# Performance work log

Hardware: AMD Instinct MI355X
Metric: run time of the kernel (lower is better)

## Reference

```python
import jax, jax.numpy as jnp
import numpy as np

C = 256

def conv1x1(x, w, b):
    # pointwise Conv3d(kernel=1): out-channel d from in-channel c
    return jnp.einsum('blhwc,dc->blhwd', x, w) + b

def setup_inputs() -> dict:
    key = jax.random.key(0)
    ks = jax.random.split(key, 20)
    inp = {
        'x': jax.random.normal(ks[0], (2, 8, 64, 64, C + 3), jnp.float32),
        'mask': jnp.ones((2, 8, 64, 64), dtype=bool),
        'spatial_correction_matrix': jax.random.normal(ks[1], (2, 8, 4, 4), jnp.float32),
    }
    scale = 1.0 / np.sqrt(C)
    names = ['sq', 'sk', 'sv', 'tq', 'tk', 'tv']
    for i, n in enumerate(names):
        inp[n + '_w'] = jax.random.normal(ks[2 + 2 * i], (C, C), jnp.float32) * scale
        inp[n + '_b'] = jax.random.normal(ks[3 + 2 * i], (C,), jnp.float32) * 0.01
    inp['s_gamma'] = jax.random.normal(ks[14], (1,), jnp.float32) * 0.1
    inp['t_gamma'] = jax.random.normal(ks[15], (1,), jnp.float32) * 0.1
    return inp

def reference(x, mask, spatial_correction_matrix,
              sq_w, sq_b, sk_w, sk_b, sv_w, sv_b, s_gamma,
              tq_w, tq_b, tk_w, tk_b, tv_w, tv_b, t_gamma):
    x_s = x[..., :-3]                      # (B,L,H,W,C)
    B, L, H, W, Ch = x_s.shape
    prev = x_s                             # last_time == None -> last_time = x.detach()
    HW = H * W

    # ---- SpatialAttention: channel-attention (CxC) per (B,L) slice ----
    q = jnp.transpose(conv1x1(x_s, sq_w, sq_b), (0, 1, 4, 2, 3)).reshape(B * L, Ch, HW)
    k = jnp.transpose(conv1x1(x_s, sk_w, sk_b), (0, 1, 4, 2, 3)).reshape(B * L, Ch, HW)
    attn = jax.nn.softmax(jnp.einsum('bcs,bds->bcd', q, k), axis=-1)   # (BL,C,C)
    v = jnp.transpose(conv1x1(x_s, sv_w, sv_b), (0, 1, 4, 2, 3)).reshape(B * L, Ch, HW)
    out = jnp.einsum('bds,bcd->bsc', v, attn).reshape(B, L, H, W, Ch)
    x1 = s_gamma * out + x_s

    # ---- TemporalAttention: query from x1, key/value from prev ----
    q2 = jnp.transpose(conv1x1(x1, tq_w, tq_b), (0, 1, 4, 2, 3)).reshape(B * L, Ch, HW)
    # key: permute(0,2,1,4,3) swaps H/W before flatten (faithful to source)
    k2 = jnp.transpose(conv1x1(prev, tk_w, tk_b), (0, 1, 4, 3, 2)).reshape(B * L, Ch, HW)
    attn2 = jax.nn.softmax(jnp.einsum('bcs,bds->bcd', q2, k2), axis=-1)
    # value: reshape of (B,C,L,H,W)-contiguous tensor into (B*L,C,HW) scrambles C/L (faithful)
    v2 = jnp.transpose(conv1x1(prev, tv_w, tv_b), (0, 4, 1, 2, 3)).reshape(B * L, Ch, HW)
    out2 = jnp.einsum('bds,bcd->bsc', v2, attn2).reshape(B, L, H, W, Ch)
    x2 = t_gamma * out2 + x1
    return x2
```

## Files before the change

### kernel.cpp

```cpp
#include <hip/hip_runtime.h>
#include <stdint.h>


#define S4 4096
#define CH 256

typedef __attribute__((ext_vector_type(8))) short bf16x8;
typedef __attribute__((ext_vector_type(4))) float f32x4;

static __device__ __forceinline__ float bf2f(unsigned short u){
  union { unsigned int i; float f; } v; v.i = ((unsigned int)u) << 16; return v.f;
}
static __device__ __forceinline__ unsigned short f2bf(float f){
  union { float f; unsigned int i; } v; v.f = f;
  unsigned int x = v.i;
  x += 0x7fffu + ((x >> 16) & 1u);
  return (unsigned short)(x >> 16);
}
static __device__ __forceinline__ void gload16(const void* g, void* l){
  __builtin_amdgcn_global_load_lds((const __attribute__((address_space(1))) void*)g,
                                   (__attribute__((address_space(3))) void*)l, 16, 0, 0);
}


__global__ void k_xprep(const float* __restrict__ x,
                        unsigned short* __restrict__ xhi,
                        unsigned short* __restrict__ xlo){
  int row = blockIdx.x;
  int c   = threadIdx.x;
  float v = x[(size_t)row*259 + c];
  unsigned short h = f2bf(v);
  xhi[(size_t)row*256 + c] = h;
  xlo[(size_t)row*256 + c] = f2bf(v - bf2f(h));
}

__global__ void k_wprep(const float* __restrict__ w0, const float* __restrict__ w1,
                        const float* __restrict__ w2, const float* __restrict__ w3,
                        const float* __restrict__ w4, const float* __restrict__ w5,
                        unsigned short* __restrict__ whi, unsigned short* __restrict__ wlo,
                        unsigned short* __restrict__ wvthi, unsigned short* __restrict__ wvtlo){
  int i = blockIdx.x*256 + threadIdx.x;
  int mat = i >> 16; int off = i & 65535;
  if (mat < 6){
    const float* src = mat==0?w0:mat==1?w1:mat==2?w2:mat==3?w3:mat==4?w4:w5;
    float v = src[off];
    unsigned short h = f2bf(v);
    whi[i] = h;
    wlo[i] = f2bf(v - bf2f(h));
  } else {
    int e = off >> 8, d = off & 255;
    float v = w2[d*256 + e];
    unsigned short h = f2bf(v);
    wvthi[off] = h;
    wvtlo[off] = f2bf(v - bf2f(h));
  }
}


__global__ void k_colsum(const float* __restrict__ x, float* __restrict__ ups){
  int bl = blockIdx.x, ch = blockIdx.y, e = threadIdx.x;
  float s = 0.f;
  for (int i=0;i<128;++i){
    int row = bl*4096 + ch*128 + i;
    s += x[(size_t)row*259 + e];
  }
  ups[(bl*32 + ch)*256 + e] = s;
}

__global__ void k_vecfin(const float* __restrict__ ups, float* __restrict__ u){
  int bl = blockIdx.x, e = threadIdx.x;
  float s = 0.f;
  for (int ch=0;ch<32;++ch) s += ups[(bl*32+ch)*256 + e];
  u[bl*256 + e] = s;
}

__global__ void k_vecs1(const float* __restrict__ sq_w, const float* __restrict__ sq_b,
                        const float* __restrict__ sk_w, const float* __restrict__ tk_w,
                        const float* __restrict__ u,
                        float* __restrict__ wqu, float* __restrict__ wku, float* __restrict__ wtku){
  int bl = blockIdx.x, mat = blockIdx.y;
  const float* W = mat==0? sq_w : mat==1? sk_w : tk_w;
  int l = threadIdx.x & 63, w = threadIdx.x >> 6;
  const float* ub = u + bl*256;
  for (int i=0;i<64;++i){
    int c = w*64 + i;
    float s = 0.f;
    #pragma unroll
    for (int j=0;j<4;++j) s += W[c*256 + l + 64*j] * ub[l + 64*j];
    #pragma unroll
    for (int off=32; off; off>>=1) s += __shfl_xor(s, off, 64);
    if (l==0){
      if (mat==0) wqu [bl*256+c] = s + 4096.f*sq_b[c];
      else if (mat==1) wku [bl*256+c] = s;
      else wtku[bl*256+c] = s;
    }
  }
}

__global__ void k_vecs2a(const unsigned short* __restrict__ a1hi, const unsigned short* __restrict__ a1lo,
                         const float* __restrict__ bv, const float* __restrict__ M1,
                         const float* __restrict__ u,
                         float* __restrict__ c1, float* __restrict__ m1u){
  int bl = blockIdx.x, mat = blockIdx.y;
  int l = threadIdx.x & 63, w = threadIdx.x >> 6;
  for (int i=0;i<64;++i){
    int c = w*64 + i;
    float s = 0.f;
    if (mat==0){
      #pragma unroll
      for (int j=0;j<4;++j){
        long o = (long)bl*65536 + c*256 + l + 64*j;
        s += (bf2f(a1hi[o]) + bf2f(a1lo[o])) * bv[l + 64*j];
      }
    } else {
      #pragma unroll
      for (int j=0;j<4;++j)
        s += M1[(long)bl*65536 + c*256 + l + 64*j] * u[bl*256 + l + 64*j];
    }
    #pragma unroll
    for (int off=32; off; off>>=1) s += __shfl_xor(s, off, 64);
    if (l==0){
      if (mat==0) c1 [bl*256+c] = s;
      else        m1u[bl*256+c] = s;
    }
  }
}

__global__ void k_vecs2b(const float* __restrict__ u, const float* __restrict__ m1u,
                         const float* __restrict__ c1, const float* __restrict__ s_g,
                         const float* __restrict__ tq_w, const float* __restrict__ tq_b,
                         float* __restrict__ b1eff, float* __restrict__ wtqh){
  __shared__ float h1[256];
  int bl = blockIdx.x, tid = threadIdx.x;
  float g = s_g[0];
  float b1 = g * c1[bl*256 + tid];
  b1eff[bl*256 + tid] = b1;
  h1[tid] = u[bl*256+tid] + g*m1u[bl*256+tid] + 4096.f*b1;
  __syncthreads();
  int l = tid & 63, w = tid >> 6;
  for (int i=0;i<64;++i){
    int c = w*64 + i;
    float s = 0.f;
    #pragma unroll
    for (int j=0;j<4;++j) s += tq_w[c*256 + l + 64*j] * h1[l + 64*j];
    #pragma unroll
    for (int off=32; off; off>>=1) s += __shfl_xor(s, off, 64);
    if (l==0) wtqh[bl*256+c] = s + 4096.f*tq_b[c];
  }
}

__global__ void k_w1eff(const float* __restrict__ M1, const float* __restrict__ s_g,
                        unsigned short* __restrict__ w1hi, unsigned short* __restrict__ w1lo){
  int bl = blockIdx.y;
  int idx = blockIdx.x*256 + threadIdx.x;
  int c = idx >> 8, e = idx & 255;
  float v = ((c==e)?1.f:0.f) + s_g[0]*M1[(long)bl*65536 + idx];
  unsigned short h = f2bf(v);
  w1hi[(long)bl*65536 + idx] = h;
  w1lo[(long)bl*65536 + idx] = f2bf(v - bf2f(h));
}

__global__ void k_gcomb(const float* __restrict__ Gp,
                        unsigned short* __restrict__ ghi, unsigned short* __restrict__ glo){
  int bl = blockIdx.y;
  int idx = blockIdx.x*256 + threadIdx.x;
  float s = 0.f;
  #pragma unroll
  for (int p=0;p<4;++p) s += Gp[(long)(bl*4+p)*65536 + idx];
  unsigned short h = f2bf(s);
  ghi[(long)bl*65536 + idx] = h;
  glo[(long)bl*65536 + idx] = f2bf(s - bf2f(h));
}

template<int MODE>
__global__ void k_softmax(const float* __restrict__ lp, const float* __restrict__ gp,
                          unsigned short* __restrict__ ahi, unsigned short* __restrict__ alo){
  int tid = threadIdx.x;
  int l = tid & 63, w = tid >> 6;
  int row = blockIdx.x*4 + w;
  int bl = row >> 8, c = row & 255;
  const float* b0 = lp + (long)bl*65536 + c*256 + l*4;
  float4 v = *(const float4*)b0;
  float m = fmaxf(fmaxf(v.x,v.y), fmaxf(v.z,v.w));
  #pragma unroll
  for (int off=32; off; off>>=1) m = fmaxf(m, __shfl_xor(m, off, 64));
  float e0=__expf(v.x-m), e1=__expf(v.y-m), e2=__expf(v.z-m), e3=__expf(v.w-m);
  float s = e0+e1+e2+e3;
  #pragma unroll
  for (int off=32; off; off>>=1) s += __shfl_xor(s, off, 64);
  float inv = 1.f/s;
  if (MODE==1) inv *= gp[0];
  float p[4] = {e0*inv, e1*inv, e2*inv, e3*inv};
  long o = (long)bl*65536 + c*256 + l*4;
  ushort4 hh;
  hh.x=f2bf(p[0]); hh.y=f2bf(p[1]); hh.z=f2bf(p[2]); hh.w=f2bf(p[3]);
  *(ushort4*)(ahi + o) = hh;
  if (MODE==0){
    ushort4 ll;
    ll.x=f2bf(p[0]-bf2f(hh.x)); ll.y=f2bf(p[1]-bf2f(hh.y));
    ll.z=f2bf(p[2]-bf2f(hh.z)); ll.w=f2bf(p[3]-bf2f(hh.w));
    *(ushort4*)(alo + o) = ll;
  }
}


template<bool SPLIT,int OUT_MODE>
__global__ __launch_bounds__(256) void k_gemm(
  const unsigned short* __restrict__ Ahi, const unsigned short* __restrict__ Alo,
  long Abl, int Ars,
  const unsigned short* __restrict__ Bhi, const unsigned short* __restrict__ Blo,
  long Bbl, int Brs,
  const float* __restrict__ bias,
  const float* __restrict__ r1a, int r1as, const float* __restrict__ r1b, int r1bs,
  const float* __restrict__ r2a, int r2as, const float* __restrict__ r2b, int r2bs,
  unsigned short* __restrict__ O16a, unsigned short* __restrict__ O16b,
  float* __restrict__ O32, long Obl, int Ors)
{
  constexpr int LDSZ = SPLIT ? 65536 : 32768;
  __shared__ char lds[LDSZ];
  char* ldsAh = lds;
  char* ldsAl = lds + 16384;
  char* ldsBh = lds + (SPLIT ? 32768 : 16384);
  char* ldsBl = lds + 49152;

  const int tid = threadIdx.x;
  const int l   = tid & 63;
  const int wid = tid >> 6;
  const int wm  = wid >> 1, wn = wid & 1;
  const int lm  = l & 15, lk = l >> 4;
  const int fm  = wm*64, fn = wn*64;
  const int bl  = blockIdx.z;
  const int m0  = blockIdx.x * 128;
  const int n0  = blockIdx.y * 128;

  f32x4 acc[4][4];
  #pragma unroll
  for (int i=0;i<4;++i)
    #pragma unroll
    for (int j=0;j<4;++j) acc[i][j] = (f32x4){0.f,0.f,0.f,0.f};

  for (int kt = 0; kt < 4; ++kt) {
    const int kq = kt << 6;
    #pragma unroll
    for (int it=0; it<4; ++it) {
      int idx = it*256 + tid;
      int r = idx >> 3;
      int kb = ((idx & 7) << 4) ^ ((r & 7) << 4);
      long ga = (long)bl*Abl + (long)(m0 + r)*Ars + kq + (kb >> 1);
      gload16(Ahi + ga, ldsAh + idx*16);
      if (SPLIT) gload16(Alo + ga, ldsAl + idx*16);
      long gb = (long)bl*Bbl + (long)(n0 + r)*Brs + kq + (kb >> 1);
      gload16(Bhi + gb, ldsBh + idx*16);
      if (SPLIT) gload16(Blo + gb, ldsBl + idx*16);
    }
    __syncthreads();
    #pragma unroll
    for (int kk=0; kk<2; ++kk) {
      bf16x8 ah[4], al_[4];
      #pragma unroll
      for (int i=0;i<4;++i) {
        int r = fm + i*16 + lm;
        int kb = ((kk<<6) + (lk<<4)) ^ ((r & 7) << 4);
        ah[i] = *(const bf16x8*)(ldsAh + r*128 + kb);
        if (SPLIT) al_[i] = *(const bf16x8*)(ldsAl + r*128 + kb);
      }
      #pragma unroll
      for (int j=0;j<4;++j) {
        int r = fn + j*16 + lm;
        int kb = ((kk<<6) + (lk<<4)) ^ ((r & 7) << 4);
        bf16x8 bh = *(const bf16x8*)(ldsBh + r*128 + kb);
        bf16x8 bl8;
        if (SPLIT) bl8 = *(const bf16x8*)(ldsBl + r*128 + kb);
        #pragma unroll
        for (int i=0;i<4;++i) {
          acc[i][j] = __builtin_amdgcn_mfma_f32_16x16x32_bf16(ah[i], bh, acc[i][j], 0, 0, 0);
          if (SPLIT) {
            acc[i][j] = __builtin_amdgcn_mfma_f32_16x16x32_bf16(ah[i], bl8, acc[i][j], 0, 0, 0);
            acc[i][j] = __builtin_amdgcn_mfma_f32_16x16x32_bf16(al_[i], bh, acc[i][j], 0, 0, 0);
          }
        }
      }
    }
    __syncthreads();
  }

  float* ldsF = (float*)lds;
  #pragma unroll
  for (int chv=0; chv<4; ++chv) {
    __syncthreads();
    if (wm == (chv >> 1)) {
      #pragma unroll
      for (int i2=0;i2<2;++i2) {
        int i = (chv & 1)*2 + i2;
        #pragma unroll
        for (int j=0;j<4;++j) {
          int n = fn + j*16 + lm;
          int m2 = i2*16 + lk*4;
          #pragma unroll
          for (int r2=0;r2<4;++r2) ldsF[(m2+r2)*136 + n] = acc[i][j][r2];
        }
      }
    }
    __syncthreads();
    #pragma unroll
    for (int g2=0; g2<2; ++g2) {
      int t2 = g2*256 + tid;
      int rr = t2 >> 4;
      int co = (t2 & 15) * 8;
      float v[8];
      #pragma unroll
      for (int e=0;e<8;++e) v[e] = ldsF[rr*136 + co + e];
      int mg = m0 + chv*32 + rr;
      int ng = n0 + co;
      long oidx = (long)bl*Obl + (long)mg*Ors + ng;
      if (OUT_MODE==0 || OUT_MODE==5){
        if (r1a){
          float a1 = r1a[bl*r1as + mg];
          #pragma unroll
          for (int e=0;e<8;++e) v[e] += a1 * r1b[bl*r1bs + ng + e];
        }
        if (r2a){
          float a2 = r2a[bl*r2as + mg];
          #pragma unroll
          for (int e=0;e<8;++e) v[e] += a2 * r2b[bl*r2bs + ng + e];
        }
      }
      if (OUT_MODE==2 || OUT_MODE==5){
        float4 o0, o1;
        o0.x=v[0]; o0.y=v[1]; o0.z=v[2]; o0.w=v[3];
        o1.x=v[4]; o1.y=v[5]; o1.z=v[6]; o1.w=v[7];
        *(float4*)(O32 + oidx)     = o0;
        *(float4*)(O32 + oidx + 4) = o1;
      } else {
        if (OUT_MODE==1){
          float b = bias ? bias[mg] : 0.f;
          #pragma unroll
          for (int e=0;e<8;++e) v[e] += b;
        }
        union { int4 vv; unsigned short u[8]; } hh, ll;
        #pragma unroll
        for (int e=0;e<8;++e) hh.u[e] = f2bf(v[e]);
        *(int4*)(O16a + oidx) = hh.vv;
        if (OUT_MODE==0){
          #pragma unroll
          for (int e=0;e<8;++e) ll.u[e] = f2bf(v[e] - bf2f(hh.u[e]));
          *(int4*)(O16b + oidx) = ll.vv;
        }
      }
    }
  }
}


template<bool BSWAP>
__global__ __launch_bounds__(256) void k_gram(
  const unsigned short* __restrict__ Xhi, const unsigned short* __restrict__ Xlo,
  float* __restrict__ Gp)
{
  __shared__ char lds[65536];
  char* ldsAh = lds;
  char* ldsAl = lds + 16384;
  char* ldsBh = lds + 32768;
  char* ldsBl = lds + 49152;

  const int tid = threadIdx.x;
  const int l = tid & 63, wid = tid >> 6;
  const int wm = wid >> 1, wn = wid & 1;
  const int lm = l & 15, lk = l >> 4;
  const int fm = wm*64, fn = wn*64;
  const int z = blockIdx.z, bl = z >> 2, sp = z & 3;
  const int m0 = blockIdx.x*128, n0 = blockIdx.y*128;
  const long Xoff = (long)bl * (4096*256);

  f32x4 acc[4][4];
  #pragma unroll
  for (int i=0;i<4;++i)
    #pragma unroll
    for (int j=0;j<4;++j) acc[i][j] = (f32x4){0.f,0.f,0.f,0.f};

  for (int kt=0; kt<16; ++kt) {
    const int k0 = sp*1024 + kt*64;
    #pragma unroll
    for (int it=0; it<4; ++it) {
      int idx = it*256 + tid;
      int s = idx & 63, ch = idx >> 6;
      int sa = k0 + s;
      int sb = BSWAP ? (((sa & 63) << 6) | (sa >> 6)) : sa;
      long gaA = Xoff + (long)sa*256 + m0 + ch*8;
      long gaB = Xoff + (long)sb*256 + n0 + ch*8;
      union { int4 v; unsigned short u[8]; } vh, vl, wh, wl;
      vh.v = *(const int4*)(Xhi + gaA);
      vl.v = *(const int4*)(Xlo + gaA);
      wh.v = *(const int4*)(Xhi + gaB);
      wl.v = *(const int4*)(Xlo + gaB);
      #pragma unroll
      for (int j=0;j<8;++j) {
        int e = ch*8 + j;
        int bo = e*128 + ((s*2) ^ ((e&7)<<4));
        *(unsigned short*)(ldsAh + bo) = vh.u[j];
        *(unsigned short*)(ldsAl + bo) = vl.u[j];
        *(unsigned short*)(ldsBh + bo) = wh.u[j];
        *(unsigned short*)(ldsBl + bo) = wl.u[j];
      }
    }
    __syncthreads();
    #pragma unroll
    for (int kk=0; kk<2; ++kk) {
      bf16x8 ah[4], al_[4];
      #pragma unroll
      for (int i=0;i<4;++i) {
        int r = fm + i*16 + lm;
        int kb = ((kk<<6) + (lk<<4)) ^ ((r & 7) << 4);
        ah[i]  = *(const bf16x8*)(ldsAh + r*128 + kb);
        al_[i] = *(const bf16x8*)(ldsAl + r*128 + kb);
      }
      #pragma unroll
      for (int j=0;j<4;++j) {
        int r = fn + j*16 + lm;
        int kb = ((kk<<6) + (lk<<4)) ^ ((r & 7) << 4);
        bf16x8 bh  = *(const bf16x8*)(ldsBh + r*128 + kb);
        bf16x8 bl8 = *(const bf16x8*)(ldsBl + r*128 + kb);
        #pragma unroll
        for (int i=0;i<4;++i) {
          acc[i][j] = __builtin_amdgcn_mfma_f32_16x16x32_bf16(ah[i], bh, acc[i][j], 0, 0, 0);
          acc[i][j] = __builtin_amdgcn_mfma_f32_16x16x32_bf16(ah[i], bl8, acc[i][j], 0, 0, 0);
          acc[i][j] = __builtin_amdgcn_mfma_f32_16x16x32_bf16(al_[i], bh, acc[i][j], 0, 0, 0);
        }
      }
    }
    __syncthreads();
  }

  float* ldsF = (float*)lds;
  #pragma unroll
  for (int chv=0; chv<4; ++chv) {
    __syncthreads();
    if (wm == (chv >> 1)) {
      #pragma unroll
      for (int i2=0;i2<2;++i2) {
        int i = (chv & 1)*2 + i2;
        #pragma unroll
        for (int j=0;j<4;++j) {
          int n = fn + j*16 + lm;
          int m2 = i2*16 + lk*4;
          #pragma unroll
          for (int r2=0;r2<4;++r2) ldsF[(m2+r2)*136 + n] = acc[i][j][r2];
        }
      }
    }
    __syncthreads();
    #pragma unroll
    for (int g2=0; g2<2; ++g2) {
      int t2 = g2*256 + tid;
      int rr = t2 >> 4;
      int co = (t2 & 15) * 8;
      int mg = m0 + chv*32 + rr;
      int ng = n0 + co;
      long oidx = (long)z*65536 + (long)mg*256 + ng;
      float4 o0, o1;
      o0.x = ldsF[rr*136+co+0]; o0.y = ldsF[rr*136+co+1];
      o0.z = ldsF[rr*136+co+2]; o0.w = ldsF[rr*136+co+3];
      o1.x = ldsF[rr*136+co+4]; o1.y = ldsF[rr*136+co+5];
      o1.z = ldsF[rr*136+co+6]; o1.w = ldsF[rr*136+co+7];
      *(float4*)(Gp + oidx)     = o0;
      *(float4*)(Gp + oidx + 4) = o1;
    }
  }
}


__global__ __launch_bounds__(256,2) void k_final(
  const unsigned short* __restrict__ v2T,
  const unsigned short* __restrict__ attn2g,
  const unsigned short* __restrict__ Xhi, const unsigned short* __restrict__ Xlo,
  const unsigned short* __restrict__ W1hi, const unsigned short* __restrict__ W1lo,
  const float* __restrict__ b1eff,
  float* __restrict__ out)
{
  __shared__ char lds[32768];
  char* ldsA = lds; char* ldsB = lds + 16384;
  const int tid = threadIdx.x;
  const int l = tid & 63, wid = tid >> 6;
  const int wm = wid >> 1, wn = wid & 1;
  const int lm = l & 15, lk = l >> 4;
  const int fm = wm*64, fn = wn*64;
  const int bl = blockIdx.z;
  const int m0 = blockIdx.x*128;
  const int n0 = blockIdx.y*128;

  f32x4 acc[4][4];
  #pragma unroll
  for (int i=0;i<4;++i)
    #pragma unroll
    for (int j=0;j<4;++j) acc[i][j] = (f32x4){0.f,0.f,0.f,0.f};

  for (int kt=0; kt<16; ++kt) {
    const int ph = kt >> 2;
    const int kq = (kt & 3) << 6;
    if (ph == 0) {
      #pragma unroll
      for (int it=0; it<4; ++it) {
        int cid = it*256 + tid;
        int d = cid & 63, sc = cid >> 6;
        int dg = kq + d;
        long row = (long)(((bl >> 3)*8 + (dg & 7))*256 + ((bl & 7) << 5) + (dg >> 3));
        union { int4 v; unsigned short u[8]; } ldv;
        ldv.v = *(const int4*)(v2T + row*4096 + m0 + sc*8);
        #pragma unroll
        for (int e=0;e<8;++e) {
          int sl = sc*8 + e;
          int bo = sl*128 + ((d*2) ^ ((sl & 7) << 4));
          *(unsigned short*)(ldsA + bo) = ldv.u[e];
        }
      }
      #pragma unroll
      for (int it=0; it<4; ++it) {
        int idx = it*256 + tid;
        int r = idx >> 3;
        int kb = ((idx & 7) << 4) ^ ((r & 7) << 4);
        long gb = (long)bl*65536 + (long)(n0 + r)*256 + kq + (kb >> 1);
        gload16(attn2g + gb, ldsB + idx*16);
      }
    } else {
      const unsigned short* As = (ph==3) ? Xlo : Xhi;
      const unsigned short* Bs = (ph==2) ? W1lo : W1hi;
      #pragma unroll
      for (int it=0; it<4; ++it) {
        int idx = it*256 + tid;
        int r = idx >> 3;
        int kb = ((idx & 7) << 4) ^ ((r & 7) << 4);
        long ga = (long)bl*1048576 + (long)(m0 + r)*256 + kq + (kb >> 1);
        gload16(As + ga, ldsA + idx*16);
        long gb = (long)bl*65536 + (long)(n0 + r)*256 + kq + (kb >> 1);
        gload16(Bs + gb, ldsB + idx*16);
      }
    }
    __syncthreads();
    #pragma unroll
    for (int kk=0; kk<2; ++kk) {
      bf16x8 a_[4];
      #pragma unroll
      for (int i=0;i<4;++i) {
        int r = fm + i*16 + lm;
        int kb = ((kk<<6) + (lk<<4)) ^ ((r & 7) << 4);
        a_[i] = *(const bf16x8*)(ldsA + r*128 + kb);
      }
      #pragma unroll
      for (int j=0;j<4;++j) {
        int r = fn + j*16 + lm;
        int kb = ((kk<<6) + (lk<<4)) ^ ((r & 7) << 4);
        bf16x8 b_ = *(const bf16x8*)(ldsB + r*128 + kb);
        #pragma unroll
        for (int i=0;i<4;++i)
          acc[i][j] = __builtin_amdgcn_mfma_f32_16x16x32_bf16(a_[i], b_, acc[i][j], 0, 0, 0);
      }
    }
    __syncthreads();
  }

  float* ldsF = (float*)lds;
  #pragma unroll
  for (int chv=0; chv<4; ++chv) {
    __syncthreads();
    if (wm == (chv >> 1)) {
      #pragma unroll
      for (int i2=0;i2<2;++i2) {
        int i = (chv & 1)*2 + i2;
        #pragma unroll
        for (int j=0;j<4;++j) {
          int n = fn + j*16 + lm;
          int m2 = i2*16 + lk*4;
          #pragma unroll
          for (int r2=0;r2<4;++r2) ldsF[(m2+r2)*136 + n] = acc[i][j][r2];
        }
      }
    }
    __syncthreads();
    #pragma unroll
    for (int g2=0; g2<2; ++g2) {
      int t2 = g2*256 + tid;
      int rr = t2 >> 4;
      int co = (t2 & 15) * 8;
      int mg = m0 + chv*32 + rr;
      int ng = n0 + co;
      long oidx = (long)bl*1048576 + (long)mg*256 + ng;
      float4 o0, o1;
      o0.x = ldsF[rr*136+co+0] + b1eff[bl*256+ng+0];
      o0.y = ldsF[rr*136+co+1] + b1eff[bl*256+ng+1];
      o0.z = ldsF[rr*136+co+2] + b1eff[bl*256+ng+2];
      o0.w = ldsF[rr*136+co+3] + b1eff[bl*256+ng+3];
      o1.x = ldsF[rr*136+co+4] + b1eff[bl*256+ng+4];
      o1.y = ldsF[rr*136+co+5] + b1eff[bl*256+ng+5];
      o1.z = ldsF[rr*136+co+6] + b1eff[bl*256+ng+6];
      o1.w = ldsF[rr*136+co+7] + b1eff[bl*256+ng+7];
      *(float4*)(out + oidx)     = o0;
      *(float4*)(out + oidx + 4) = o1;
    }
  }
}


extern "C" void kernel_launch(void* const* d_in, const int* in_sizes, int n_in,
                              void* d_out, int out_size, void* d_ws, size_t ws_size,
                              hipStream_t stream)
{
  const float* x    = (const float*)d_in[0];
  const float* sq_w = (const float*)d_in[3];
  const float* sq_b = (const float*)d_in[4];
  const float* sk_w = (const float*)d_in[5];
  const float* sk_b = (const float*)d_in[6];
  const float* sv_w = (const float*)d_in[7];
  const float* sv_b = (const float*)d_in[8];
  const float* tq_w = (const float*)d_in[9];
  const float* tq_b = (const float*)d_in[10];
  const float* tk_w = (const float*)d_in[11];
  const float* tk_b = (const float*)d_in[12];
  const float* tv_w = (const float*)d_in[13];
  const float* tv_b = (const float*)d_in[14];
  const float* s_g  = (const float*)d_in[15];
  const float* t_g  = (const float*)d_in[16];

  char* p = (char*)d_ws;
  size_t off = 0;
  auto take = [&](size_t n){ char* r = p + off; off = (off + n + 255) & ~(size_t)255; return r; };

  unsigned short* Whi    = (unsigned short*)take((size_t)6*65536*2);
  unsigned short* Wlo    = (unsigned short*)take((size_t)6*65536*2);
  unsigned short* WvThi  = (unsigned short*)take((size_t)65536*2);
  unsigned short* WvTlo  = (unsigned short*)take((size_t)65536*2);
  unsigned short* Xhi    = (unsigned short*)take((size_t)16*S4*CH*2);
  unsigned short* Xlo    = (unsigned short*)take((size_t)16*S4*CH*2);
  unsigned short* v2T    = (unsigned short*)take((size_t)16*S4*CH*2);
  float*          Gp     = (float*)take((size_t)64*65536*4);
  unsigned short* G1hi   = (unsigned short*)take((size_t)16*65536*2);
  unsigned short* G1lo   = (unsigned short*)take((size_t)16*65536*2);
  unsigned short* GShi   = (unsigned short*)take((size_t)16*65536*2);
  unsigned short* GSlo   = (unsigned short*)take((size_t)16*65536*2);
  unsigned short* Pthi   = (unsigned short*)take((size_t)16*65536*2);
  unsigned short* Ptlo   = (unsigned short*)take((size_t)16*65536*2);
  unsigned short* G2hi   = (unsigned short*)take((size_t)16*65536*2);
  unsigned short* G2lo   = (unsigned short*)take((size_t)16*65536*2);
  unsigned short* W1hi   = (unsigned short*)take((size_t)16*65536*2);
  unsigned short* W1lo   = (unsigned short*)take((size_t)16*65536*2);
  unsigned short* a1hi   = (unsigned short*)take((size_t)16*65536*2);
  unsigned short* a1lo   = (unsigned short*)take((size_t)16*65536*2);
  unsigned short* a2g    = (unsigned short*)take((size_t)16*65536*2);
  float*          M1     = (float*)take((size_t)16*65536*4);
  float*          logits = (float*)take((size_t)16*65536*4);
  float*          ups    = (float*)take((size_t)16*32*256*4);
  float*          u      = (float*)take((size_t)16*256*4);
  float*          wqu    = (float*)take((size_t)16*256*4);
  float*          wku    = (float*)take((size_t)16*256*4);
  float*          wtku   = (float*)take((size_t)16*256*4);
  float*          c1     = (float*)take((size_t)16*256*4);
  float*          m1u    = (float*)take((size_t)16*256*4);
  float*          b1eff  = (float*)take((size_t)16*256*4);
  float*          wtqh   = (float*)take((size_t)16*256*4);

  const long XBL = (long)S4*CH;
  const long GBL = 65536;

  k_wprep<<<dim3(1792), 256, 0, stream>>>(sq_w, sk_w, sv_w, tq_w, tk_w, tv_w,
                                          Whi, Wlo, WvThi, WvTlo);
  k_xprep<<<dim3(65536), 256, 0, stream>>>(x, Xhi, Xlo);

  k_gram<false><<<dim3(2,2,64), 256, 0, stream>>>(Xhi, Xlo, Gp);
  k_gcomb<<<dim3(256,16), 256, 0, stream>>>(Gp, G1hi, G1lo);
  k_gram<true><<<dim3(2,2,64), 256, 0, stream>>>(Xhi, Xlo, Gp);
  k_gcomb<<<dim3(256,16), 256, 0, stream>>>(Gp, GShi, GSlo);

  k_colsum<<<dim3(16,32), 256, 0, stream>>>(x, ups);
  k_vecfin<<<dim3(16), 256, 0, stream>>>(ups, u);
  k_vecs1<<<dim3(16,3), 256, 0, stream>>>(sq_w, sq_b, sk_w, tk_w, u, wqu, wku, wtku);

  k_gemm<true,0><<<dim3(2,2,16), 256, 0, stream>>>(
     Whi+1*65536, Wlo+1*65536, 0, 256,  G1hi, G1lo, GBL, 256,
     nullptr, nullptr,0,nullptr,0, nullptr,0,nullptr,0,
     Pthi, Ptlo, nullptr, GBL, 256);
  k_gemm<true,5><<<dim3(2,2,16), 256, 0, stream>>>(
     Whi+0*65536, Wlo+0*65536, 0, 256,  Pthi, Ptlo, GBL, 256,
     nullptr, wqu,256, sk_b,0,  sq_b,0, wku,256,
     nullptr, nullptr, logits, GBL, 256);
  k_softmax<0><<<dim3(1024), 256, 0, stream>>>(logits, nullptr, a1hi, a1lo);

  k_gemm<true,2><<<dim3(2,2,16), 256, 0, stream>>>(
     a1hi, a1lo, GBL, 256,  WvThi, WvTlo, 0, 256,
     nullptr, nullptr,0,nullptr,0, nullptr,0,nullptr,0,
     nullptr, nullptr, M1, GBL, 256);
  k_w1eff<<<dim3(256,16), 256, 0, stream>>>(M1, s_g, W1hi, W1lo);
  k_vecs2a<<<dim3(16,2), 256, 0, stream>>>(a1hi, a1lo, sv_b, M1, u, c1, m1u);
  k_vecs2b<<<dim3(16), 256, 0, stream>>>(u, m1u, c1, s_g, tq_w, tq_b, b1eff, wtqh);

  k_gemm<true,0><<<dim3(2,2,16), 256, 0, stream>>>(
     W1hi, W1lo, GBL, 256,  GShi, GSlo, GBL, 256,
     nullptr, b1eff,256, u,256,  nullptr,0,nullptr,0,
     G2hi, G2lo, nullptr, GBL, 256);
  k_gemm<true,0><<<dim3(2,2,16), 256, 0, stream>>>(
     Whi+4*65536, Wlo+4*65536, 0, 256,  G2hi, G2lo, GBL, 256,
     nullptr, nullptr,0,nullptr,0, nullptr,0,nullptr,0,
     Pthi, Ptlo, nullptr, GBL, 256);
  k_gemm<true,5><<<dim3(2,2,16), 256, 0, stream>>>(
     Whi+3*65536, Wlo+3*65536, 0, 256,  Pthi, Ptlo, GBL, 256,
     nullptr, wtqh,256, tk_b,0,  tq_b,0, wtku,256,
     nullptr, nullptr, logits, GBL, 256);
  k_softmax<1><<<dim3(1024), 256, 0, stream>>>(logits, t_g, a2g, nullptr);

  k_gemm<false,1><<<dim3(2,32,16), 256, 0, stream>>>(
     Whi+5*65536, nullptr, 0, 256,  Xhi, nullptr, XBL, 256,
     tv_b, nullptr,0,nullptr,0, nullptr,0,nullptr,0,
     v2T, nullptr, nullptr, XBL, S4);

  k_final<<<dim3(32,2,16), 256, 0, stream>>>(v2T, a2g, Xhi, Xlo, W1hi, W1lo, b1eff, (float*)d_out);
}
```

Baseline: 577.8 us.

## Fuse small per-slice GEMM/softmax chain into one megakernel and fuse colsum into xprep

Replaces the chain of small 256x256 GEMMs, softmaxes and vector kernels with a single k_mega launch that runs one 512-thread block per (B,L) slice. The column sum is folded into the x bf16-split prep kernel, which now handles 64 rows per block. The Gram kernel's split-K goes from 4 to 8 with a remapped block order and vectorised LDS transposes. The aim is to cut launch overhead and the intermediate global round-trips, but the megakernel only uses 16 blocks, which may leave most CUs idle.

```diff
diff --git a/kernel.cpp b/kernel.cpp
--- a/kernel.cpp
+++ b/kernel.cpp
@@ -23,15 +23,30 @@
 }
 
 
-__global__ void k_xprep(const float* __restrict__ x,
-                        unsigned short* __restrict__ xhi,
-                        unsigned short* __restrict__ xlo){
-  int row = blockIdx.x;
+__global__ void k_xprep2(const float* __restrict__ x,
+                         unsigned short* __restrict__ xhi,
+                         unsigned short* __restrict__ xlo,
+                         float* __restrict__ ups){
+  int blk = blockIdx.x;
   int c   = threadIdx.x;
-  float v = x[(size_t)row*259 + c];
-  unsigned short h = f2bf(v);
-  xhi[(size_t)row*256 + c] = h;
-  xlo[(size_t)row*256 + c] = f2bf(v - bf2f(h));
+  long rbase = (long)blk * 64;
+  float s = 0.f;
+  for (int i = 0; i < 64; ++i){
+    long row = rbase + i;
+    float v = x[row*259 + c];
+    unsigned short h = f2bf(v);
+    xhi[row*256 + c] = h;
+    xlo[row*256 + c] = f2bf(v - bf2f(h));
+    s += v;
+  }
+  ups[(long)blk*256 + c] = s;
+}
+
+__global__ void k_vecfin(const float* __restrict__ ups, float* __restrict__ u){
+  int bl = blockIdx.x, e = threadIdx.x;
+  float s = 0.f;
+  for (int ch = 0; ch < 64; ++ch) s += ups[(long)(bl*64 + ch)*256 + e];
+  u[bl*256 + e] = s;
 }
 
 __global__ void k_wprep(const float* __restrict__ w0, const float* __restrict__ w1,
@@ -56,299 +71,16 @@
   }
 }
 
-
-__global__ void k_colsum(const float* __restrict__ x, float* __restrict__ ups){
-  int bl = blockIdx.x, ch = blockIdx.y, e = threadIdx.x;
-  float s = 0.f;
-  for (int i=0;i<128;++i){
-    int row = bl*4096 + ch*128 + i;
-    s += x[(size_t)row*259 + e];
-  }
-  ups[(bl*32 + ch)*256 + e] = s;
-}
-
-__global__ void k_vecfin(const float* __restrict__ ups, float* __restrict__ u){
-  int bl = blockIdx.x, e = threadIdx.x;
-  float s = 0.f;
-  for (int ch=0;ch<32;++ch) s += ups[(bl*32+ch)*256 + e];
-  u[bl*256 + e] = s;
-}
-
-__global__ void k_vecs1(const float* __restrict__ sq_w, const float* __restrict__ sq_b,
-                        const float* __restrict__ sk_w, const float* __restrict__ tk_w,
-                        const float* __restrict__ u,
-                        float* __restrict__ wqu, float* __restrict__ wku, float* __restrict__ wtku){
-  int bl = blockIdx.x, mat = blockIdx.y;
-  const float* W = mat==0? sq_w : mat==1? sk_w : tk_w;
-  int l = threadIdx.x & 63, w = threadIdx.x >> 6;
-  const float* ub = u + bl*256;
-  for (int i=0;i<64;++i){
-    int c = w*64 + i;
-    float s = 0.f;
-    #pragma unroll
-    for (int j=0;j<4;++j) s += W[c*256 + l + 64*j] * ub[l + 64*j];
-    #pragma unroll
-    for (int off=32; off; off>>=1) s += __shfl_xor(s, off, 64);
-    if (l==0){
-      if (mat==0) wqu [bl*256+c] = s + 4096.f*sq_b[c];
-      else if (mat==1) wku [bl*256+c] = s;
-      else wtku[bl*256+c] = s;
-    }
-  }
-}
-
-__global__ void k_vecs2a(const unsigned short* __restrict__ a1hi, const unsigned short* __restrict__ a1lo,
-                         const float* __restrict__ bv, const float* __restrict__ M1,
-                         const float* __restrict__ u,
-                         float* __restrict__ c1, float* __restrict__ m1u){
-  int bl = blockIdx.x, mat = blockIdx.y;
-  int l = threadIdx.x & 63, w = threadIdx.x >> 6;
-  for (int i=0;i<64;++i){
-    int c = w*64 + i;
-    float s = 0.f;
-    if (mat==0){
-      #pragma unroll
-      for (int j=0;j<4;++j){
-        long o = (long)bl*65536 + c*256 + l + 64*j;
-        s += (bf2f(a1hi[o]) + bf2f(a1lo[o])) * bv[l + 64*j];
-      }
-    } else {
-      #pragma unroll
-      for (int j=0;j<4;++j)
-        s += M1[(long)bl*65536 + c*256 + l + 64*j] * u[bl*256 + l + 64*j];
-    }
-    #pragma unroll
-    for (int off=32; off; off>>=1) s += __shfl_xor(s, off, 64);
-    if (l==0){
-      if (mat==0) c1 [bl*256+c] = s;
-      else        m1u[bl*256+c] = s;
-    }
-  }
-}
-
-__global__ void k_vecs2b(const float* __restrict__ u, const float* __restrict__ m1u,
-                         const float* __restrict__ c1, const float* __restrict__ s_g,
-                         const float* __restrict__ tq_w, const float* __restrict__ tq_b,
-                         float* __restrict__ b1eff, float* __restrict__ wtqh){
-  __shared__ float h1[256];
-  int bl = blockIdx.x, tid = threadIdx.x;
-  float g = s_g[0];
-  float b1 = g * c1[bl*256 + tid];
-  b1eff[bl*256 + tid] = b1;
-  h1[tid] = u[bl*256+tid] + g*m1u[bl*256+tid] + 4096.f*b1;
-  __syncthreads();
-  int l = tid & 63, w = tid >> 6;
-  for (int i=0;i<64;++i){
-    int c = w*64 + i;
-    float s = 0.f;
-    #pragma unroll
-    for (int j=0;j<4;++j) s += tq_w[c*256 + l + 64*j] * h1[l + 64*j];
-    #pragma unroll
-    for (int off=32; off; off>>=1) s += __shfl_xor(s, off, 64);
-    if (l==0) wtqh[bl*256+c] = s + 4096.f*tq_b[c];
-  }
-}
-
-__global__ void k_w1eff(const float* __restrict__ M1, const float* __restrict__ s_g,
-                        unsigned short* __restrict__ w1hi, unsigned short* __restrict__ w1lo){
-  int bl = blockIdx.y;
-  int idx = blockIdx.x*256 + threadIdx.x;
-  int c = idx >> 8, e = idx & 255;
-  float v = ((c==e)?1.f:0.f) + s_g[0]*M1[(long)bl*65536 + idx];
-  unsigned short h = f2bf(v);
-  w1hi[(long)bl*65536 + idx] = h;
-  w1lo[(long)bl*65536 + idx] = f2bf(v - bf2f(h));
-}
-
 __global__ void k_gcomb(const float* __restrict__ Gp,
                         unsigned short* __restrict__ ghi, unsigned short* __restrict__ glo){
   int bl = blockIdx.y;
   int idx = blockIdx.x*256 + threadIdx.x;
   float s = 0.f;
   #pragma unroll
-  for (int p=0;p<4;++p) s += Gp[(long)(bl*4+p)*65536 + idx];
+  for (int p = 0; p < 8; ++p) s += Gp[(long)(bl*8 + p)*65536 + idx];
   unsigned short h = f2bf(s);
   ghi[(long)bl*65536 + idx] = h;
   glo[(long)bl*65536 + idx] = f2bf(s - bf2f(h));
-}
-
-template<int MODE>
-__global__ void k_softmax(const float* __restrict__ lp, const float* __restrict__ gp,
-                          unsigned short* __restrict__ ahi, unsigned short* __restrict__ alo){
-  int tid = threadIdx.x;
-  int l = tid & 63, w = tid >> 6;
-  int row = blockIdx.x*4 + w;
-  int bl = row >> 8, c = row & 255;
-  const float* b0 = lp + (long)bl*65536 + c*256 + l*4;
-  float4 v = *(const float4*)b0;
-  float m = fmaxf(fmaxf(v.x,v.y), fmaxf(v.z,v.w));
-  #pragma unroll
-  for (int off=32; off; off>>=1) m = fmaxf(m, __shfl_xor(m, off, 64));
-  float e0=__expf(v.x-m), e1=__expf(v.y-m), e2=__expf(v.z-m), e3=__expf(v.w-m);
-  float s = e0+e1+e2+e3;
-  #pragma unroll
-  for (int off=32; off; off>>=1) s += __shfl_xor(s, off, 64);
-  float inv = 1.f/s;
-  if (MODE==1) inv *= gp[0];
-  float p[4] = {e0*inv, e1*inv, e2*inv, e3*inv};
-  long o = (long)bl*65536 + c*256 + l*4;
-  ushort4 hh;
-  hh.x=f2bf(p[0]); hh.y=f2bf(p[1]); hh.z=f2bf(p[2]); hh.w=f2bf(p[3]);
-  *(ushort4*)(ahi + o) = hh;
-  if (MODE==0){
-    ushort4 ll;
-    ll.x=f2bf(p[0]-bf2f(hh.x)); ll.y=f2bf(p[1]-bf2f(hh.y));
-    ll.z=f2bf(p[2]-bf2f(hh.z)); ll.w=f2bf(p[3]-bf2f(hh.w));
-    *(ushort4*)(alo + o) = ll;
-  }
-}
-
-
-template<bool SPLIT,int OUT_MODE>
-__global__ __launch_bounds__(256) void k_gemm(
-  const unsigned short* __restrict__ Ahi, const unsigned short* __restrict__ Alo,
-  long Abl, int Ars,
-  const unsigned short* __restrict__ Bhi, const unsigned short* __restrict__ Blo,
-  long Bbl, int Brs,
-  const float* __restrict__ bias,
-  const float* __restrict__ r1a, int r1as, const float* __restrict__ r1b, int r1bs,
-  const float* __restrict__ r2a, int r2as, const float* __restrict__ r2b, int r2bs,
-  unsigned short* __restrict__ O16a, unsigned short* __restrict__ O16b,
-  float* __restrict__ O32, long Obl, int Ors)
-{
-  constexpr int LDSZ = SPLIT ? 65536 : 32768;
-  __shared__ char lds[LDSZ];
-  char* ldsAh = lds;
-  char* ldsAl = lds + 16384;
-  char* ldsBh = lds + (SPLIT ? 32768 : 16384);
-  char* ldsBl = lds + 49152;
-
-  const int tid = threadIdx.x;
-  const int l   = tid & 63;
-  const int wid = tid >> 6;
-  const int wm  = wid >> 1, wn = wid & 1;
-  const int lm  = l & 15, lk = l >> 4;
-  const int fm  = wm*64, fn = wn*64;
-  const int bl  = blockIdx.z;
-  const int m0  = blockIdx.x * 128;
-  const int n0  = blockIdx.y * 128;
-
-  f32x4 acc[4][4];
-  #pragma unroll
-  for (int i=0;i<4;++i)
-    #pragma unroll
-    for (int j=0;j<4;++j) acc[i][j] = (f32x4){0.f,0.f,0.f,0.f};
-
-  for (int kt = 0; kt < 4; ++kt) {
-    const int kq = kt << 6;
-    #pragma unroll
-    for (int it=0; it<4; ++it) {
-      int idx = it*256 + tid;
-      int r = idx >> 3;
-      int kb = ((idx & 7) << 4) ^ ((r & 7) << 4);
-      long ga = (long)bl*Abl + (long)(m0 + r)*Ars + kq + (kb >> 1);
-      gload16(Ahi + ga, ldsAh + idx*16);
-      if (SPLIT) gload16(Alo + ga, ldsAl + idx*16);
-      long gb = (long)bl*Bbl + (long)(n0 + r)*Brs + kq + (kb >> 1);
-      gload16(Bhi + gb, ldsBh + idx*16);
-      if (SPLIT) gload16(Blo + gb, ldsBl + idx*16);
-    }
-    __syncthreads();
-    #pragma unroll
-    for (int kk=0; kk<2; ++kk) {
-      bf16x8 ah[4], al_[4];
-      #pragma unroll
-      for (int i=0;i<4;++i) {
-        int r = fm + i*16 + lm;
-        int kb = ((kk<<6) + (lk<<4)) ^ ((r & 7) << 4);
-        ah[i] = *(const bf16x8*)(ldsAh + r*128 + kb);
-        if (SPLIT) al_[i] = *(const bf16x8*)(ldsAl + r*128 + kb);
-      }
-      #pragma unroll
-      for (int j=0;j<4;++j) {
-        int r = fn + j*16 + lm;
-        int kb = ((kk<<6) + (lk<<4)) ^ ((r & 7) << 4);
-        bf16x8 bh = *(const bf16x8*)(ldsBh + r*128 + kb);
-        bf16x8 bl8;
-        if (SPLIT) bl8 = *(const bf16x8*)(ldsBl + r*128 + kb);
-        #pragma unroll
-        for (int i=0;i<4;++i) {
-          acc[i][j] = __builtin_amdgcn_mfma_f32_16x16x32_bf16(ah[i], bh, acc[i][j], 0, 0, 0);
-          if (SPLIT) {
-            acc[i][j] = __builtin_amdgcn_mfma_f32_16x16x32_bf16(ah[i], bl8, acc[i][j], 0, 0, 0);
-            acc[i][j] = __builtin_amdgcn_mfma_f32_16x16x32_bf16(al_[i], bh, acc[i][j], 0, 0, 0);
-          }
-        }
-      }
-    }
-    __syncthreads();
-  }
-
-  float* ldsF = (float*)lds;
-  #pragma unroll
-  for (int chv=0; chv<4; ++chv) {
-    __syncthreads();
-    if (wm == (chv >> 1)) {
-      #pragma unroll
-      for (int i2=0;i2<2;++i2) {
-        int i = (chv & 1)*2 + i2;
-        #pragma unroll
-        for (int j=0;j<4;++j) {
-          int n = fn + j*16 + lm;
-          int m2 = i2*16 + lk*4;
-          #pragma unroll
-          for (int r2=0;r2<4;++r2) ldsF[(m2+r2)*136 + n] = acc[i][j][r2];
-        }
-      }
-    }
-    __syncthreads();
-    #pragma unroll
-    for (int g2=0; g2<2; ++g2) {
-      int t2 = g2*256 + tid;
-      int rr = t2 >> 4;
-      int co = (t2 & 15) * 8;
-      float v[8];
-      #pragma unroll
-      for (int e=0;e<8;++e) v[e] = ldsF[rr*136 + co + e];
-      int mg = m0 + chv*32 + rr;
-      int ng = n0 + co;
-      long oidx = (long)bl*Obl + (long)mg*Ors + ng;
-      if (OUT_MODE==0 || OUT_MODE==5){
-        if (r1a){
-          float a1 = r1a[bl*r1as + mg];
-          #pragma unroll
-          for (int e=0;e<8;++e) v[e] += a1 * r1b[bl*r1bs + ng + e];
-        }
-        if (r2a){
-          float a2 = r2a[bl*r2as + mg];
-          #pragma unroll
-          for (int e=0;e<8;++e) v[e] += a2 * r2b[bl*r2bs + ng + e];
-        }
-      }
-      if (OUT_MODE==2 || OUT_MODE==5){
-        float4 o0, o1;
-        o0.x=v[0]; o0.y=v[1]; o0.z=v[2]; o0.w=v[3];
-        o1.x=v[4]; o1.y=v[5]; o1.z=v[6]; o1.w=v[7];
-        *(float4*)(O32 + oidx)     = o0;
-        *(float4*)(O32 + oidx + 4) = o1;
-      } else {
-        if (OUT_MODE==1){
-          float b = bias ? bias[mg] : 0.f;
-          #pragma unroll
-          for (int e=0;e<8;++e) v[e] += b;
-        }
-        union { int4 vv; unsigned short u[8]; } hh, ll;
-        #pragma unroll
-        for (int e=0;e<8;++e) hh.u[e] = f2bf(v[e]);
-        *(int4*)(O16a + oidx) = hh.vv;
-        if (OUT_MODE==0){
-          #pragma unroll
-          for (int e=0;e<8;++e) ll.u[e] = f2bf(v[e] - bf2f(hh.u[e]));
-          *(int4*)(O16b + oidx) = ll.vv;
-        }
-      }
-    }
-  }
 }
 
 
@@ -368,9 +100,17 @@
   const int wm = wid >> 1, wn = wid & 1;
   const int lm = l & 15, lk = l >> 4;
   const int fm = wm*64, fn = wn*64;
-  const int z = blockIdx.z, bl = z >> 2, sp = z & 3;
-  const int m0 = blockIdx.x*128, n0 = blockIdx.y*128;
+
+  int flat = blockIdx.x + 2*(blockIdx.y + 2*blockIdx.z);
+  int lg = (flat & 7)*64 + (flat >> 3);
+  const int m0 = (lg & 1)*128;
+  const int n0 = ((lg >> 1) & 1)*128;
+  const int zz = lg >> 2;
+  const int bl = zz >> 3, sp = zz & 7;
   const long Xoff = (long)bl * (4096*256);
+
+  const int sg = tid & 15;
+  const int eg = tid >> 4;
 
   f32x4 acc[4][4];
   #pragma unroll
@@ -378,50 +118,55 @@
     #pragma unroll
     for (int j=0;j<4;++j) acc[i][j] = (f32x4){0.f,0.f,0.f,0.f};
 
-  for (int kt=0; kt<16; ++kt) {
-    const int k0 = sp*1024 + kt*64;
-    #pragma unroll
-    for (int it=0; it<4; ++it) {
-      int idx = it*256 + tid;
-      int s = idx & 63, ch = idx >> 6;
-      int sa = k0 + s;
+  union U4 { int4 v; unsigned short u[8]; };
+
+  for (int kt = 0; kt < 8; ++kt){
+    const int k0 = sp*512 + kt*64;
+    U4 va[4], vla[4], vb[4], vlb[4];
+    #pragma unroll
+    for (int ss = 0; ss < 4; ++ss){
+      int sa = k0 + sg*4 + ss;
       int sb = BSWAP ? (((sa & 63) << 6) | (sa >> 6)) : sa;
-      long gaA = Xoff + (long)sa*256 + m0 + ch*8;
-      long gaB = Xoff + (long)sb*256 + n0 + ch*8;
-      union { int4 v; unsigned short u[8]; } vh, vl, wh, wl;
-      vh.v = *(const int4*)(Xhi + gaA);
-      vl.v = *(const int4*)(Xlo + gaA);
-      wh.v = *(const int4*)(Xhi + gaB);
-      wl.v = *(const int4*)(Xlo + gaB);
-      #pragma unroll
-      for (int j=0;j<8;++j) {
-        int e = ch*8 + j;
-        int bo = e*128 + ((s*2) ^ ((e&7)<<4));
-        *(unsigned short*)(ldsAh + bo) = vh.u[j];
-        *(unsigned short*)(ldsAl + bo) = vl.u[j];
-        *(unsigned short*)(ldsBh + bo) = wh.u[j];
-        *(unsigned short*)(ldsBl + bo) = wl.u[j];
-      }
-    }
-    __syncthreads();
-    #pragma unroll
-    for (int kk=0; kk<2; ++kk) {
+      long gaA = Xoff + (long)sa*256 + m0 + eg*8;
+      long gaB = Xoff + (long)sb*256 + n0 + eg*8;
+      va[ss].v  = *(const int4*)(Xhi + gaA);
+      vla[ss].v = *(const int4*)(Xlo + gaA);
+      vb[ss].v  = *(const int4*)(Xhi + gaB);
+      vlb[ss].v = *(const int4*)(Xlo + gaB);
+    }
+    #pragma unroll
+    for (int j = 0; j < 8; ++j){
+      int e_loc = eg*8 + j;
+      int bo = e_loc*128 + ((sg*8) ^ (j << 4));
+      ushort4 t;
+      t.x=va[0].u[j];  t.y=va[1].u[j];  t.z=va[2].u[j];  t.w=va[3].u[j];
+      *(ushort4*)(ldsAh + bo) = t;
+      t.x=vla[0].u[j]; t.y=vla[1].u[j]; t.z=vla[2].u[j]; t.w=vla[3].u[j];
+      *(ushort4*)(ldsAl + bo) = t;
+      t.x=vb[0].u[j];  t.y=vb[1].u[j];  t.z=vb[2].u[j];  t.w=vb[3].u[j];
+      *(ushort4*)(ldsBh + bo) = t;
+      t.x=vlb[0].u[j]; t.y=vlb[1].u[j]; t.z=vlb[2].u[j]; t.w=vlb[3].u[j];
+      *(ushort4*)(ldsBl + bo) = t;
+    }
+    __syncthreads();
+    #pragma unroll
+    for (int kk = 0; kk < 2; ++kk){
       bf16x8 ah[4], al_[4];
       #pragma unroll
-      for (int i=0;i<4;++i) {
+      for (int i=0;i<4;++i){
         int r = fm + i*16 + lm;
         int kb = ((kk<<6) + (lk<<4)) ^ ((r & 7) << 4);
         ah[i]  = *(const bf16x8*)(ldsAh + r*128 + kb);
         al_[i] = *(const bf16x8*)(ldsAl + r*128 + kb);
       }
       #pragma unroll
-      for (int j=0;j<4;++j) {
+      for (int j=0;j<4;++j){
         int r = fn + j*16 + lm;
         int kb = ((kk<<6) + (lk<<4)) ^ ((r & 7) << 4);
         bf16x8 bh  = *(const bf16x8*)(ldsBh + r*128 + kb);
         bf16x8 bl8 = *(const bf16x8*)(ldsBl + r*128 + kb);
         #pragma unroll
-        for (int i=0;i<4;++i) {
+        for (int i=0;i<4;++i){
           acc[i][j] = __builtin_amdgcn_mfma_f32_16x16x32_bf16(ah[i], bh, acc[i][j], 0, 0, 0);
           acc[i][j] = __builtin_amdgcn_mfma_f32_16x16x32_bf16(ah[i], bl8, acc[i][j], 0, 0, 0);
           acc[i][j] = __builtin_amdgcn_mfma_f32_16x16x32_bf16(al_[i], bh, acc[i][j], 0, 0, 0);
@@ -433,14 +178,14 @@
 
   float* ldsF = (float*)lds;
   #pragma unroll
-  for (int chv=0; chv<4; ++chv) {
-    __syncthreads();
-    if (wm == (chv >> 1)) {
-      #pragma unroll
-      for (int i2=0;i2<2;++i2) {
+  for (int chv = 0; chv < 4; ++chv){
+    __syncthreads();
+    if (wm == (chv >> 1)){
+      #pragma unroll
+      for (int i2=0;i2<2;++i2){
         int i = (chv & 1)*2 + i2;
         #pragma unroll
-        for (int j=0;j<4;++j) {
+        for (int j=0;j<4;++j){
           int n = fn + j*16 + lm;
           int m2 = i2*16 + lk*4;
           #pragma unroll
@@ -450,13 +195,13 @@
     }
     __syncthreads();
     #pragma unroll
-    for (int g2=0; g2<2; ++g2) {
+    for (int g2 = 0; g2 < 2; ++g2){
       int t2 = g2*256 + tid;
       int rr = t2 >> 4;
       int co = (t2 & 15) * 8;
       int mg = m0 + chv*32 + rr;
       int ng = n0 + co;
-      long oidx = (long)z*65536 + (long)mg*256 + ng;
+      long oidx = (long)zz*65536 + (long)mg*256 + ng;
       float4 o0, o1;
       o0.x = ldsF[rr*136+co+0]; o0.y = ldsF[rr*136+co+1];
       o0.z = ldsF[rr*136+co+2]; o0.w = ldsF[rr*136+co+3];
@@ -464,6 +209,455 @@
       o1.z = ldsF[rr*136+co+6]; o1.w = ldsF[rr*136+co+7];
       *(float4*)(Gp + oidx)     = o0;
       *(float4*)(Gp + oidx + 4) = o1;
+    }
+  }
+}
+
+
+__device__ __forceinline__ void mega_tile(
+  char* lds, int tid,
+  const unsigned short* __restrict__ Ah, const unsigned short* __restrict__ Al,
+  const unsigned short* __restrict__ Bh, const unsigned short* __restrict__ Bl,
+  f32x4 acc[4][4])
+{
+  char* ldsAh = lds;
+  char* ldsAl = lds + 32768;
+  char* ldsBh = lds + 65536;
+  char* ldsBl = lds + 81920;
+  const int l = tid & 63, wid = tid >> 6;
+  const int g = wid >> 2, w2 = wid & 3;
+  const int wm = w2 >> 1, wn = w2 & 1;
+  const int lm = l & 15, lk = l >> 4;
+  const int fm = g*128 + wm*64, fn = wn*64;
+
+  for (int kt = 0; kt < 4; ++kt){
+    const int kq = kt << 6;
+    #pragma unroll
+    for (int it = 0; it < 4; ++it){
+      int idx = it*512 + tid;
+      int r = idx >> 3;
+      int kb = ((idx & 7) << 4) ^ ((r & 7) << 4);
+      long ga = (long)r*256 + kq + (kb >> 1);
+      gload16(Ah + ga, ldsAh + idx*16);
+      gload16(Al + ga, ldsAl + idx*16);
+    }
+    #pragma unroll
+    for (int it = 0; it < 2; ++it){
+      int idx = it*512 + tid;
+      int r = idx >> 3;
+      int kb = ((idx & 7) << 4) ^ ((r & 7) << 4);
+      long gb = (long)r*256 + kq + (kb >> 1);
+      gload16(Bh + gb, ldsBh + idx*16);
+      gload16(Bl + gb, ldsBl + idx*16);
+    }
+    __syncthreads();
+    #pragma unroll
+    for (int kk = 0; kk < 2; ++kk){
+      bf16x8 ah[4], al_[4];
+      #pragma unroll
+      for (int i=0;i<4;++i){
+        int r = fm + i*16 + lm;
+        int kb = ((kk<<6) + (lk<<4)) ^ ((r & 7) << 4);
+        ah[i]  = *(const bf16x8*)(ldsAh + r*128 + kb);
+        al_[i] = *(const bf16x8*)(ldsAl + r*128 + kb);
+      }
+      #pragma unroll
+      for (int j=0;j<4;++j){
+        int r = fn + j*16 + lm;
+        int kb = ((kk<<6) + (lk<<4)) ^ ((r & 7) << 4);
+        bf16x8 bh  = *(const bf16x8*)(ldsBh + r*128 + kb);
+        bf16x8 bl8 = *(const bf16x8*)(ldsBl + r*128 + kb);
+        #pragma unroll
+        for (int i=0;i<4;++i){
+          acc[i][j] = __builtin_amdgcn_mfma_f32_16x16x32_bf16(ah[i], bh, acc[i][j], 0, 0, 0);
+          acc[i][j] = __builtin_amdgcn_mfma_f32_16x16x32_bf16(ah[i], bl8, acc[i][j], 0, 0, 0);
+          acc[i][j] = __builtin_amdgcn_mfma_f32_16x16x32_bf16(al_[i], bh, acc[i][j], 0, 0, 0);
+        }
+      }
+    }
+    __syncthreads();
+  }
+}
+
+template<int MODE>
+__device__ __forceinline__ void mega_epi(
+  char* lds, int tid, f32x4 acc[4][4], int bl, int n0, float gs,
+  const float* ra1, const float* rb1, const float* ra2, const float* rb2,
+  const float* pu, float* ph1,
+  unsigned short* __restrict__ Oh, unsigned short* __restrict__ Ol,
+  float* __restrict__ O32)
+{
+  const int l = tid & 63, wid = tid >> 6;
+  const int g = wid >> 2, w2 = wid & 3;
+  const int wm = w2 >> 1, wn = w2 & 1;
+  const int lm = l & 15, lk = l >> 4;
+  const int fnl = wn*64;
+  float* ldsF = (float*)(lds + g*17408);
+  const int tid2 = tid & 255;
+  const int gr = tid >> 8;
+
+  #pragma unroll
+  for (int chv = 0; chv < 4; ++chv){
+    __syncthreads();
+    if (wm == (chv >> 1)){
+      #pragma unroll
+      for (int i2=0;i2<2;++i2){
+        int i = (chv & 1)*2 + i2;
+        #pragma unroll
+        for (int j=0;j<4;++j){
+          int n = fnl + j*16 + lm;
+          int m2 = i2*16 + lk*4;
+          #pragma unroll
+          for (int r2=0;r2<4;++r2) ldsF[(m2+r2)*136 + n] = acc[i][j][r2];
+        }
+      }
+    }
+    __syncthreads();
+    float* ldsFr = (float*)(lds + gr*17408);
+    #pragma unroll
+    for (int g2 = 0; g2 < 2; ++g2){
+      int t2 = g2*256 + tid2;
+      int rr = t2 >> 4;
+      int co = (t2 & 15) * 8;
+      float v[8];
+      #pragma unroll
+      for (int e=0;e<8;++e) v[e] = ldsFr[rr*136 + co + e];
+      int mg = gr*128 + chv*32 + rr;
+      int ng = n0 + co;
+      long oidx = (long)bl*65536 + (long)mg*256 + ng;
+      if (MODE == 1){
+        float a1v = ra1[mg], a2v = ra2[mg];
+        #pragma unroll
+        for (int e=0;e<8;++e) v[e] += a1v*rb1[ng+e] + a2v*rb2[ng+e];
+        float4 o0, o1;
+        o0.x=v[0]; o0.y=v[1]; o0.z=v[2]; o0.w=v[3];
+        o1.x=v[4]; o1.y=v[5]; o1.z=v[6]; o1.w=v[7];
+        *(float4*)(O32 + oidx)     = o0;
+        *(float4*)(O32 + oidx + 4) = o1;
+      } else {
+        if (MODE == 2){
+          float hs = 0.f;
+          #pragma unroll
+          for (int e=0;e<8;++e){
+            float w = ((mg == ng + e) ? 1.f : 0.f) + gs*v[e];
+            hs += w * pu[ng+e];
+            v[e] = w;
+          }
+          atomicAdd(&ph1[mg], hs);
+        }
+        if (MODE == 3){
+          float a1v = ra1[mg];
+          #pragma unroll
+          for (int e=0;e<8;++e) v[e] += a1v * rb1[ng+e];
+        }
+        union { int4 vv; unsigned short u[8]; } hh, ll;
+        #pragma unroll
+        for (int e=0;e<8;++e) hh.u[e] = f2bf(v[e]);
+        *(int4*)(Oh + oidx) = hh.vv;
+        #pragma unroll
+        for (int e=0;e<8;++e) ll.u[e] = f2bf(v[e] - bf2f(hh.u[e]));
+        *(int4*)(Ol + oidx) = ll.vv;
+      }
+    }
+  }
+  __threadfence();
+  __syncthreads();
+}
+
+template<int SMODE>
+__device__ __forceinline__ void mega_softmax(
+  int bl, int tid, const float* __restrict__ logits, float tg,
+  const float* psvb, float* pc1,
+  unsigned short* __restrict__ Oh, unsigned short* __restrict__ Ol)
+{
+  const int l = tid & 63, wid = tid >> 6;
+  const long base = (long)bl*65536;
+  for (int rr = 0; rr < 32; rr += 2){
+    int c0 = wid*32 + rr;
+    const float* p0 = logits + base + (long)c0*256 + l*4;
+    float4 va = *(const float4*)p0;
+    float4 vb = *(const float4*)(p0 + 256);
+    float ma = fmaxf(fmaxf(va.x,va.y), fmaxf(va.z,va.w));
+    float mb = fmaxf(fmaxf(vb.x,vb.y), fmaxf(vb.z,vb.w));
+    #pragma unroll
+    for (int off=32; off; off>>=1){
+      ma = fmaxf(ma, __shfl_xor(ma, off, 64));
+      mb = fmaxf(mb, __shfl_xor(mb, off, 64));
+    }
+    float ea0=__expf(va.x-ma), ea1=__expf(va.y-ma), ea2=__expf(va.z-ma), ea3=__expf(va.w-ma);
+    float eb0=__expf(vb.x-mb), eb1=__expf(vb.y-mb), eb2=__expf(vb.z-mb), eb3=__expf(vb.w-mb);
+    float sa = ea0+ea1+ea2+ea3, sb = eb0+eb1+eb2+eb3;
+    float da = 0.f, db = 0.f;
+    if (SMODE == 0){
+      float4 bv = *(const float4*)(psvb + l*4);
+      da = ea0*bv.x + ea1*bv.y + ea2*bv.z + ea3*bv.w;
+      db = eb0*bv.x + eb1*bv.y + eb2*bv.z + eb3*bv.w;
+    }
+    #pragma unroll
+    for (int off=32; off; off>>=1){
+      sa += __shfl_xor(sa, off, 64);
+      sb += __shfl_xor(sb, off, 64);
+      if (SMODE == 0){ da += __shfl_xor(da, off, 64); db += __shfl_xor(db, off, 64); }
+    }
+    float ia = 1.f/sa, ib = 1.f/sb;
+    if (SMODE == 1){ ia *= tg; ib *= tg; }
+    float pa0=ea0*ia, pa1=ea1*ia, pa2=ea2*ia, pa3=ea3*ia;
+    float pb0=eb0*ib, pb1v=eb1*ib, pb2=eb2*ib, pb3=eb3*ib;
+    ushort4 h0, h1v;
+    h0.x=f2bf(pa0); h0.y=f2bf(pa1); h0.z=f2bf(pa2); h0.w=f2bf(pa3);
+    h1v.x=f2bf(pb0); h1v.y=f2bf(pb1v); h1v.z=f2bf(pb2); h1v.w=f2bf(pb3);
+    *(ushort4*)(Oh + base + (long)c0*256 + l*4)     = h0;
+    *(ushort4*)(Oh + base + (long)(c0+1)*256 + l*4) = h1v;
+    if (SMODE == 0){
+      ushort4 l0, l1v;
+      l0.x=f2bf(pa0-bf2f(h0.x)); l0.y=f2bf(pa1-bf2f(h0.y));
+      l0.z=f2bf(pa2-bf2f(h0.z)); l0.w=f2bf(pa3-bf2f(h0.w));
+      l1v.x=f2bf(pb0-bf2f(h1v.x)); l1v.y=f2bf(pb1v-bf2f(h1v.y));
+      l1v.z=f2bf(pb2-bf2f(h1v.z)); l1v.w=f2bf(pb3-bf2f(h1v.w));
+      *(ushort4*)(Ol + base + (long)c0*256 + l*4)     = l0;
+      *(ushort4*)(Ol + base + (long)(c0+1)*256 + l*4) = l1v;
+      if (l == 0){ pc1[c0] = da*ia; pc1[c0+1] = db*ib; }
+    }
+  }
+}
+
+__global__ __launch_bounds__(512) void k_mega(
+  const unsigned short* __restrict__ Whi, const unsigned short* __restrict__ Wlo,
+  const unsigned short* __restrict__ WvThi, const unsigned short* __restrict__ WvTlo,
+  const unsigned short* __restrict__ G1hi, const unsigned short* __restrict__ G1lo,
+  const unsigned short* __restrict__ GShi, const unsigned short* __restrict__ GSlo,
+  const float* __restrict__ sq_w, const float* __restrict__ sk_w,
+  const float* __restrict__ tk_w, const float* __restrict__ tq_w,
+  const float* __restrict__ sq_b, const float* __restrict__ sk_b,
+  const float* __restrict__ sv_b, const float* __restrict__ tq_b,
+  const float* __restrict__ tk_b,
+  const float* __restrict__ s_gp, const float* __restrict__ t_gp,
+  const float* __restrict__ u,
+  unsigned short* __restrict__ Pth, unsigned short* __restrict__ Ptl,
+  float* __restrict__ logits,
+  unsigned short* __restrict__ a1h, unsigned short* __restrict__ a1l,
+  unsigned short* __restrict__ W1h, unsigned short* __restrict__ W1l,
+  unsigned short* __restrict__ G2h, unsigned short* __restrict__ G2l,
+  unsigned short* __restrict__ a2g,
+  float* __restrict__ b1eff_g)
+{
+  __shared__ char lds[111616];
+  float* P = (float*)(lds + 98304);
+  float* pu    = P;
+  float* psqb  = P + 256;
+  float* pskb  = P + 512;
+  float* psvb  = P + 768;
+  float* ptqb  = P + 1024;
+  float* ptkb  = P + 1280;
+  float* pwqu  = P + 1536;
+  float* pwku  = P + 1792;
+  float* pwtku = P + 2048;
+  float* pwtqh = P + 2304;
+  float* pc1   = P + 2560;
+  float* ph1   = P + 2816;
+  float* pb1   = P + 3072;
+
+  const int tid = threadIdx.x;
+  const int bl = blockIdx.x;
+  const float gs = s_gp[0], tg = t_gp[0];
+  const long gb = (long)bl*65536;
+
+  if (tid < 256){
+    pu[tid]   = u[bl*256 + tid];
+    psqb[tid] = sq_b[tid];
+    pskb[tid] = sk_b[tid];
+    psvb[tid] = sv_b[tid];
+    ptqb[tid] = tq_b[tid];
+    ptkb[tid] = tk_b[tid];
+    ph1[tid]  = 0.f;
+  }
+  __syncthreads();
+
+  {
+    int c = tid & 255, hh = tid >> 8;
+    if (hh == 0){
+      float s1 = 0.f, s2 = 0.f;
+      #pragma unroll 4
+      for (int e = 0; e < 256; e += 4){
+        float4 w1_ = *(const float4*)(sq_w + c*256 + e);
+        float4 w2_ = *(const float4*)(tk_w + c*256 + e);
+        float u0=pu[e], u1=pu[e+1], u2=pu[e+2], u3=pu[e+3];
+        s1 += w1_.x*u0 + w1_.y*u1 + w1_.z*u2 + w1_.w*u3;
+        s2 += w2_.x*u0 + w2_.y*u1 + w2_.z*u2 + w2_.w*u3;
+      }
+      pwqu[c]  = s1 + 4096.f*psqb[c];
+      pwtku[c] = s2;
+    } else {
+      float s = 0.f;
+      #pragma unroll 4
+      for (int e = 0; e < 256; e += 4){
+        float4 w1_ = *(const float4*)(sk_w + c*256 + e);
+        s += w1_.x*pu[e] + w1_.y*pu[e+1] + w1_.z*pu[e+2] + w1_.w*pu[e+3];
+      }
+      pwku[c] = s;
+    }
+    __syncthreads();
+  }
+
+  f32x4 acc[4][4];
+  #define ZACC { for (int i_=0;i_<4;++i_) for (int j_=0;j_<4;++j_) acc[i_][j_]=(f32x4){0.f,0.f,0.f,0.f}; }
+
+  for (int n0 = 0; n0 < 256; n0 += 128){
+    ZACC;
+    mega_tile(lds, tid, Whi + 65536, Wlo + 65536, G1hi + gb + n0*256, G1lo + gb + n0*256, acc);
+    mega_epi<0>(lds, tid, acc, bl, n0, 0.f, nullptr,nullptr,nullptr,nullptr, pu, ph1, Pth, Ptl, nullptr);
+  }
+  for (int n0 = 0; n0 < 256; n0 += 128){
+    ZACC;
+    mega_tile(lds, tid, Whi, Wlo, Pth + gb + n0*256, Ptl + gb + n0*256, acc);
+    mega_epi<1>(lds, tid, acc, bl, n0, 0.f, pwqu, pskb, psqb, pwku, pu, ph1, nullptr, nullptr, logits);
+  }
+  mega_softmax<0>(bl, tid, logits, 1.f, psvb, pc1, a1h, a1l);
+  __threadfence();
+  __syncthreads();
+  for (int n0 = 0; n0 < 256; n0 += 128){
+    ZACC;
+    mega_tile(lds, tid, a1h + gb, a1l + gb, WvThi + n0*256, WvTlo + n0*256, acc);
+    mega_epi<2>(lds, tid, acc, bl, n0, gs, nullptr,nullptr,nullptr,nullptr, pu, ph1, W1h, W1l, nullptr);
+  }
+  if (tid < 256){
+    float b1 = gs * pc1[tid];
+    pb1[tid] = b1;
+    b1eff_g[bl*256 + tid] = b1;
+    ph1[tid] = ph1[tid] + 4096.f*b1;
+  }
+  __syncthreads();
+  if (tid < 256){
+    int c = tid;
+    float s = 0.f;
+    #pragma unroll 4
+    for (int e = 0; e < 256; e += 4){
+      float4 w = *(const float4*)(tq_w + c*256 + e);
+      s += w.x*ph1[e] + w.y*ph1[e+1] + w.z*ph1[e+2] + w.w*ph1[e+3];
+    }
+    pwtqh[c] = s + 4096.f*ptqb[c];
+  }
+  __syncthreads();
+  for (int n0 = 0; n0 < 256; n0 += 128){
+    ZACC;
+    mega_tile(lds, tid, W1h + gb, W1l + gb, GShi + gb + n0*256, GSlo + gb + n0*256, acc);
+    mega_epi<3>(lds, tid, acc, bl, n0, 0.f, pb1, pu, nullptr, nullptr, pu, ph1, G2h, G2l, nullptr);
+  }
+  for (int n0 = 0; n0 < 256; n0 += 128){
+    ZACC;
+    mega_tile(lds, tid, Whi + 4*65536, Wlo + 4*65536, G2h + gb + n0*256, G2l + gb + n0*256, acc);
+    mega_epi<0>(lds, tid, acc, bl, n0, 0.f, nullptr,nullptr,nullptr,nullptr, pu, ph1, Pth, Ptl, nullptr);
+  }
+  for (int n0 = 0; n0 < 256; n0 += 128){
+    ZACC;
+    mega_tile(lds, tid, Whi + 3*65536, Wlo + 3*65536, Pth + gb + n0*256, Ptl + gb + n0*256, acc);
+    mega_epi<1>(lds, tid, acc, bl, n0, 0.f, pwtqh, ptkb, ptqb, pwtku, pu, ph1, nullptr, nullptr, logits);
+  }
+  mega_softmax<1>(bl, tid, logits, tg, psvb, pc1, a2g, nullptr);
+  #undef ZACC
+}
+
+
+template<bool SPLIT,int OUT_MODE>
+__global__ __launch_bounds__(256) void k_gemm(
+  const unsigned short* __restrict__ Ahi, const unsigned short* __restrict__ Alo,
+  long Abl, int Ars,
+  const unsigned short* __restrict__ Bhi, const unsigned short* __restrict__ Blo,
+  long Bbl, int Brs,
+  const float* __restrict__ bias,
+  unsigned short* __restrict__ O16a,
+  long Obl, int Ors)
+{
+  constexpr int LDSZ = 32768;
+  __shared__ char lds[LDSZ];
+  char* ldsAh = lds;
+  char* ldsBh = lds + 16384;
+
+  const int tid = threadIdx.x;
+  const int l   = tid & 63;
+  const int wid = tid >> 6;
+  const int wm  = wid >> 1, wn = wid & 1;
+  const int lm  = l & 15, lk = l >> 4;
+  const int fm  = wm*64, fn = wn*64;
+  const int bl  = blockIdx.z;
+  const int m0  = blockIdx.x * 128;
+  const int n0  = blockIdx.y * 128;
+
+  f32x4 acc[4][4];
+  #pragma unroll
+  for (int i=0;i<4;++i)
+    #pragma unroll
+    for (int j=0;j<4;++j) acc[i][j] = (f32x4){0.f,0.f,0.f,0.f};
+
+  for (int kt = 0; kt < 4; ++kt){
+    const int kq = kt << 6;
+    #pragma unroll
+    for (int it=0; it<4; ++it){
+      int idx = it*256 + tid;
+      int r = idx >> 3;
+      int kb = ((idx & 7) << 4) ^ ((r & 7) << 4);
+      long ga = (long)bl*Abl + (long)(m0 + r)*Ars + kq + (kb >> 1);
+      gload16(Ahi + ga, ldsAh + idx*16);
+      long gbb = (long)bl*Bbl + (long)(n0 + r)*Brs + kq + (kb >> 1);
+      gload16(Bhi + gbb, ldsBh + idx*16);
+    }
+    __syncthreads();
+    #pragma unroll
+    for (int kk=0; kk<2; ++kk){
+      bf16x8 ah[4];
+      #pragma unroll
+      for (int i=0;i<4;++i){
+        int r = fm + i*16 + lm;
+        int kb = ((kk<<6) + (lk<<4)) ^ ((r & 7) << 4);
+        ah[i] = *(const bf16x8*)(ldsAh + r*128 + kb);
+      }
+      #pragma unroll
+      for (int j=0;j<4;++j){
+        int r = fn + j*16 + lm;
+        int kb = ((kk<<6) + (lk<<4)) ^ ((r & 7) << 4);
+        bf16x8 bh = *(const bf16x8*)(ldsBh + r*128 + kb);
+        #pragma unroll
+        for (int i=0;i<4;++i)
+          acc[i][j] = __builtin_amdgcn_mfma_f32_16x16x32_bf16(ah[i], bh, acc[i][j], 0, 0, 0);
+      }
+    }
+    __syncthreads();
+  }
+
+  float* ldsF = (float*)lds;
+  #pragma unroll
+  for (int chv=0; chv<4; ++chv){
+    __syncthreads();
+    if (wm == (chv >> 1)){
+      #pragma unroll
+      for (int i2=0;i2<2;++i2){
+        int i = (chv & 1)*2 + i2;
+        #pragma unroll
+        for (int j=0;j<4;++j){
+          int n = fn + j*16 + lm;
+          int m2 = i2*16 + lk*4;
+          #pragma unroll
+          for (int r2=0;r2<4;++r2) ldsF[(m2+r2)*136 + n] = acc[i][j][r2];
+        }
+      }
+    }
+    __syncthreads();
+    #pragma unroll
+    for (int g2=0; g2<2; ++g2){
+      int t2 = g2*256 + tid;
+      int rr = t2 >> 4;
+      int co = (t2 & 15) * 8;
+      float v[8];
+      #pragma unroll
+      for (int e=0;e<8;++e) v[e] = ldsF[rr*136 + co + e];
+      int mg = m0 + chv*32 + rr;
+      int ng = n0 + co;
+      long oidx = (long)bl*Obl + (long)mg*Ors + ng;
+      float b = bias ? bias[mg] : 0.f;
+      union { int4 vv; unsigned short u[8]; } hh;
+      #pragma unroll
+      for (int e=0;e<8;++e) hh.u[e] = f2bf(v[e] + b);
+      *(int4*)(O16a + oidx) = hh.vv;
     }
   }
 }
@@ -494,12 +688,12 @@
     #pragma unroll
     for (int j=0;j<4;++j) acc[i][j] = (f32x4){0.f,0.f,0.f,0.f};
 
-  for (int kt=0; kt<16; ++kt) {
+  for (int kt=0; kt<16; ++kt){
     const int ph = kt >> 2;
     const int kq = (kt & 3) << 6;
-    if (ph == 0) {
-      #pragma unroll
-      for (int it=0; it<4; ++it) {
+    if (ph == 0){
+      #pragma unroll
+      for (int it=0; it<4; ++it){
         int cid = it*256 + tid;
         int d = cid & 63, sc = cid >> 6;
         int dg = kq + d;
@@ -507,46 +701,46 @@
         union { int4 v; unsigned short u[8]; } ldv;
         ldv.v = *(const int4*)(v2T + row*4096 + m0 + sc*8);
         #pragma unroll
-        for (int e=0;e<8;++e) {
+        for (int e=0;e<8;++e){
           int sl = sc*8 + e;
           int bo = sl*128 + ((d*2) ^ ((sl & 7) << 4));
           *(unsigned short*)(ldsA + bo) = ldv.u[e];
         }
       }
       #pragma unroll
-      for (int it=0; it<4; ++it) {
+      for (int it=0; it<4; ++it){
         int idx = it*256 + tid;
         int r = idx >> 3;
         int kb = ((idx & 7) << 4) ^ ((r & 7) << 4);
-        long gb = (long)bl*65536 + (long)(n0 + r)*256 + kq + (kb >> 1);
-        gload16(attn2g + gb, ldsB + idx*16);
+        long gbb = (long)bl*65536 + (long)(n0 + r)*256 + kq + (kb >> 1);
+        gload16(attn2g + gbb, ldsB + idx*16);
       }
     } else {
       const unsigned short* As = (ph==3) ? Xlo : Xhi;
       const unsigned short* Bs = (ph==2) ? W1lo : W1hi;
       #pragma unroll
-      for (int it=0; it<4; ++it) {
+      for (int it=0; it<4; ++it){
         int idx = it*256 + tid;
         int r = idx >> 3;
         int kb = ((idx & 7) << 4) ^ ((r & 7) << 4);
         long ga = (long)bl*1048576 + (long)(m0 + r)*256 + kq + (kb >> 1);
         gload16(As + ga, ldsA + idx*16);
-        long gb = (long)bl*65536 + (long)(n0 + r)*256 + kq + (kb >> 1);
-        gload16(Bs + gb, ldsB + idx*16);
-      }
-    }
-    __syncthreads();
-    #pragma unroll
-    for (int kk=0; kk<2; ++kk) {
+        long gbb = (long)bl*65536 + (long)(n0 + r)*256 + kq + (kb >> 1);
+        gload16(Bs + gbb, ldsB + idx*16);
+      }
+    }
+    __syncthreads();
+    #pragma unroll
+    for (int kk=0; kk<2; ++kk){
       bf16x8 a_[4];
       #pragma unroll
-      for (int i=0;i<4;++i) {
+      for (int i=0;i<4;++i){
         int r = fm + i*16 + lm;
         int kb = ((kk<<6) + (lk<<4)) ^ ((r & 7) << 4);
         a_[i] = *(const bf16x8*)(ldsA + r*128 + kb);
       }
       #pragma unroll
-      for (int j=0;j<4;++j) {
+      for (int j=0;j<4;++j){
         int r = fn + j*16 + lm;
         int kb = ((kk<<6) + (lk<<4)) ^ ((r & 7) << 4);
         bf16x8 b_ = *(const bf16x8*)(ldsB + r*128 + kb);
@@ -560,14 +754,14 @@
 
   float* ldsF = (float*)lds;
   #pragma unroll
-  for (int chv=0; chv<4; ++chv) {
-    __syncthreads();
-    if (wm == (chv >> 1)) {
-      #pragma unroll
-      for (int i2=0;i2<2;++i2) {
+  for (int chv=0; chv<4; ++chv){
+    __syncthreads();
+    if (wm == (chv >> 1)){
+      #pragma unroll
+      for (int i2=0;i2<2;++i2){
         int i = (chv & 1)*2 + i2;
         #pragma unroll
-        for (int j=0;j<4;++j) {
+        for (int j=0;j<4;++j){
           int n = fn + j*16 + lm;
           int m2 = i2*16 + lk*4;
           #pragma unroll
@@ -577,7 +771,7 @@
     }
     __syncthreads();
     #pragma unroll
-    for (int g2=0; g2<2; ++g2) {
+    for (int g2=0; g2<2; ++g2){
       int t2 = g2*256 + tid;
       int rr = t2 >> 4;
       int co = (t2 & 15) * 8;
@@ -631,7 +825,7 @@
   unsigned short* Xhi    = (unsigned short*)take((size_t)16*S4*CH*2);
   unsigned short* Xlo    = (unsigned short*)take((size_t)16*S4*CH*2);
   unsigned short* v2T    = (unsigned short*)take((size_t)16*S4*CH*2);
-  float*          Gp     = (float*)take((size_t)64*65536*4);
+  float*          Gp     = (float*)take((size_t)128*65536*4);
   unsigned short* G1hi   = (unsigned short*)take((size_t)16*65536*2);
   unsigned short* G1lo   = (unsigned short*)take((size_t)16*65536*2);
   unsigned short* GShi   = (unsigned short*)take((size_t)16*65536*2);
@@ -645,70 +839,32 @@
   unsigned short* a1hi   = (unsigned short*)take((size_t)16*65536*2);
   unsigned short* a1lo   = (unsigned short*)take((size_t)16*65536*2);
   unsigned short* a2g    = (unsigned short*)take((size_t)16*65536*2);
-  float*          M1     = (float*)take((size_t)16*65536*4);
   float*          logits = (float*)take((size_t)16*65536*4);
-  float*          ups    = (float*)take((size_t)16*32*256*4);
+  float*          ups    = (float*)take((size_t)1024*256*4);
   float*          u      = (float*)take((size_t)16*256*4);
-  float*          wqu    = (float*)take((size_t)16*256*4);
-  float*          wku    = (float*)take((size_t)16*256*4);
-  float*          wtku   = (float*)take((size_t)16*256*4);
-  float*          c1     = (float*)take((size_t)16*256*4);
-  float*          m1u    = (float*)take((size_t)16*256*4);
   float*          b1eff  = (float*)take((size_t)16*256*4);
-  float*          wtqh   = (float*)take((size_t)16*256*4);
 
   const long XBL = (long)S4*CH;
-  const long GBL = 65536;
 
   k_wprep<<<dim3(1792), 256, 0, stream>>>(sq_w, sk_w, sv_w, tq_w, tk_w, tv_w,
                                           Whi, Wlo, WvThi, WvTlo);
-  k_xprep<<<dim3(65536), 256, 0, stream>>>(x, Xhi, Xlo);
-
-  k_gram<false><<<dim3(2,2,64), 256, 0, stream>>>(Xhi, Xlo, Gp);
+  k_xprep2<<<dim3(1024), 256, 0, stream>>>(x, Xhi, Xlo, ups);
+  k_vecfin<<<dim3(16), 256, 0, stream>>>(ups, u);
+
+  k_gram<false><<<dim3(2,2,128), 256, 0, stream>>>(Xhi, Xlo, Gp);
   k_gcomb<<<dim3(256,16), 256, 0, stream>>>(Gp, G1hi, G1lo);
-  k_gram<true><<<dim3(2,2,64), 256, 0, stream>>>(Xhi, Xlo, Gp);
+  k_gram<true><<<dim3(2,2,128), 256, 0, stream>>>(Xhi, Xlo, Gp);
   k_gcomb<<<dim3(256,16), 256, 0, stream>>>(Gp, GShi, GSlo);
 
-  k_colsum<<<dim3(16,32), 256, 0, stream>>>(x, ups);
-  k_vecfin<<<dim3(16), 256, 0, stream>>>(ups, u);
-  k_vecs1<<<dim3(16,3), 256, 0, stream>>>(sq_w, sq_b, sk_w, tk_w, u, wqu, wku, wtku);
-
-  k_gemm<true,0><<<dim3(2,2,16), 256, 0, stream>>>(
-     Whi+1*65536, Wlo+1*65536, 0, 256,  G1hi, G1lo, GBL, 256,
-     nullptr, nullptr,0,nullptr,0, nullptr,0,nullptr,0,
-     Pthi, Ptlo, nullptr, GBL, 256);
-  k_gemm<true,5><<<dim3(2,2,16), 256, 0, stream>>>(
-     Whi+0*65536, Wlo+0*65536, 0, 256,  Pthi, Ptlo, GBL, 256,
-     nullptr, wqu,256, sk_b,0,  sq_b,0, wku,256,
-     nullptr, nullptr, logits, GBL, 256);
-  k_softmax<0><<<dim3(1024), 256, 0, stream>>>(logits, nullptr, a1hi, a1lo);
-
-  k_gemm<true,2><<<dim3(2,2,16), 256, 0, stream>>>(
-     a1hi, a1lo, GBL, 256,  WvThi, WvTlo, 0, 256,
-     nullptr, nullptr,0,nullptr,0, nullptr,0,nullptr,0,
-     nullptr, nullptr, M1, GBL, 256);
-  k_w1eff<<<dim3(256,16), 256, 0, stream>>>(M1, s_g, W1hi, W1lo);
-  k_vecs2a<<<dim3(16,2), 256, 0, stream>>>(a1hi, a1lo, sv_b, M1, u, c1, m1u);
-  k_vecs2b<<<dim3(16), 256, 0, stream>>>(u, m1u, c1, s_g, tq_w, tq_b, b1eff, wtqh);
-
-  k_gemm<true,0><<<dim3(2,2,16), 256, 0, stream>>>(
-     W1hi, W1lo, GBL, 256,  GShi, GSlo, GBL, 256,
-     nullptr, b1eff,256, u,256,  nullptr,0,nullptr,0,
-     G2hi, G2lo, nullptr, GBL, 256);
-  k_gemm<true,0><<<dim3(2,2,16), 256, 0, stream>>>(
-     Whi+4*65536, Wlo+4*65536, 0, 256,  G2hi, G2lo, GBL, 256,
-     nullptr, nullptr,0,nullptr,0, nullptr,0,nullptr,0,
-     Pthi, Ptlo, nullptr, GBL, 256);
-  k_gemm<true,5><<<dim3(2,2,16), 256, 0, stream>>>(
-     Whi+3*65536, Wlo+3*65536, 0, 256,  Pthi, Ptlo, GBL, 256,
-     nullptr, wtqh,256, tk_b,0,  tq_b,0, wtku,256,
-     nullptr, nullptr, logits, GBL, 256);
-  k_softmax<1><<<dim3(1024), 256, 0, stream>>>(logits, t_g, a2g, nullptr);
+  k_mega<<<dim3(16), 512, 0, stream>>>(
+     Whi, Wlo, WvThi, WvTlo, G1hi, G1lo, GShi, GSlo,
+     sq_w, sk_w, tk_w, tq_w, sq_b, sk_b, sv_b, tq_b, tk_b,
+     s_g, t_g, u,
+     Pthi, Ptlo, logits, a1hi, a1lo, W1hi, W1lo, G2hi, G2lo, a2g, b1eff);
 
   k_gemm<false,1><<<dim3(2,32,16), 256, 0, stream>>>(
      Whi+5*65536, nullptr, 0, 256,  Xhi, nullptr, XBL, 256,
-     tv_b, nullptr,0,nullptr,0, nullptr,0,nullptr,0,
-     v2T, nullptr, nullptr, XBL, S4);
+     tv_b, v2T, XBL, S4);
 
   k_final<<<dim3(32,2,16), 256, 0, stream>>>(v2T, a2g, Xhi, Xlo, W1hi, W1lo, b1eff, (float*)d_out);
 }
```

New measurement: 607.9 us. 1.05x slower.
